# Performance work log

Hardware: AMD Instinct MI355X
Metric: run time of the kernel (lower is better)

## Reference

```python
import jax, jax.numpy as jnp
import numpy as np

N_NODES = 50000
N_EDGES = 500000
D = 128  # node/edge feature dim


def setup_inputs() -> dict:
    key = jax.random.key(0)
    k1, k2, k3, k4, k5 = jax.random.split(key, 5)
    x_node = jax.random.normal(k1, (N_NODES, D), dtype=jnp.float32)
    x_edge = jax.random.normal(k2, (N_EDGES, D), dtype=jnp.float32)
    edge_index = jax.random.randint(k3, (N_EDGES, 2), 0, N_NODES, dtype=jnp.int64)
    # MLP params: Linear(3D -> D) -> ReLU -> Linear(D -> D)
    W1 = jax.random.normal(k4, (3 * D, D), dtype=jnp.float32) * (1.0 / np.sqrt(3 * D))
    b1 = jnp.zeros((D,), dtype=jnp.float32)
    W2 = jax.random.normal(k5, (D, D), dtype=jnp.float32) * (1.0 / np.sqrt(D))
    b2 = jnp.zeros((D,), dtype=jnp.float32)
    return {"x_node": x_node, "x_edge": x_edge, "edge_index": edge_index,
            "W1": W1, "b1": b1, "W2": W2, "b2": b2}


def reference(x_node, x_edge, edge_index, W1, b1, W2, b2):
    # gather node features at both endpoints of each edge
    v0 = x_node[edge_index[:, 0]]          # [E, D]
    v1 = x_node[edge_index[:, 1]]          # [E, D]
    x_new = jnp.concatenate([v0, v1, x_edge], axis=1)  # [E, 3D]
    h = jax.nn.relu(x_new @ W1 + b1)       # [E, D]
    x_edge_new = h @ W2 + b2               # [E, D]
    return x_edge_new
```

## Files before the change

### kernel.cpp

```cpp
#include <hip/hip_runtime.h>
#include <stdint.h>

#define D 128
#define MT 64

typedef short short8 __attribute__((ext_vector_type(8)));
typedef float f32x16 __attribute__((ext_vector_type(16)));

__device__ __forceinline__ unsigned short f2bf(float f) {
    union { float f; uint32_t u; } v;
    v.f = f;
    uint32_t u = v.u;
    uint32_t r = (u + 0x7fffu + ((u >> 16) & 1u)) >> 16;
    return (unsigned short)r;
}

__global__ void pack_weights_kernel(const float* __restrict__ W1,
                                    const float* __restrict__ W2,
                                    unsigned short* __restrict__ W1p,
                                    unsigned short* __restrict__ W2p) {
    int t = blockIdx.x * 256 + threadIdx.x;
    if (t < 6144) {
        int kt = t >> 8, nt = (t >> 6) & 3, lane = t & 63;
        int n = nt * 32 + (lane & 31);
        int kb = kt * 16 + (lane >> 5) * 8;
        unsigned short* dst = W1p + t * 8;
        #pragma unroll
        for (int j = 0; j < 8; ++j) dst[j] = f2bf(W1[(kb + j) * D + n]);
    } else if (t < 8192) {
        int u = t - 6144;
        int kt = u >> 8, nt = (u >> 6) & 3, lane = u & 63;
        int n = nt * 32 + (lane & 31);
        int kb = kt * 16 + (lane >> 5) * 8;
        unsigned short* dst = W2p + u * 8;
        #pragma unroll
        for (int j = 0; j < 8; ++j) dst[j] = f2bf(W2[(kb + j) * D + n]);
    }
}

__global__ __launch_bounds__(256, 3) void edge_mlp_kernel(
    const float* __restrict__ x_node,
    const float* __restrict__ x_edge,
    const int* __restrict__ eidx,
    const unsigned short* __restrict__ W1p,
    const unsigned short* __restrict__ W2p,
    const float* __restrict__ b1,
    const float* __restrict__ b2,
    float* __restrict__ out,
    int E) {
    __shared__ unsigned short lds[MT * 392];
    unsigned short* Hs = lds;

    const int t = threadIdx.x;
    const int r0 = blockIdx.x * MT;

    {
        const int lane32 = t & 31;
        const int rsub = t >> 5;
        #pragma unroll
        for (int rb = 0; rb < 8; ++rb) {
            int row = rb * 8 + rsub;
            int rg = r0 + row;
            int rgc = rg < E ? rg : E - 1;
            int e0 = eidx[2 * rgc];
            int e1 = eidx[2 * rgc + 1];
            float4 v0 = ((const float4*)(x_node + (size_t)e0 * D))[lane32];
            float4 v1 = ((const float4*)(x_node + (size_t)e1 * D))[lane32];
            float4 v2 = ((const float4*)(x_edge + (size_t)rgc * D))[lane32];
            unsigned short* base = &lds[row * 392 + lane32 * 4];
            ushort4 p;
            p.x = f2bf(v0.x); p.y = f2bf(v0.y); p.z = f2bf(v0.z); p.w = f2bf(v0.w);
            *(ushort4*)(base) = p;
            p.x = f2bf(v1.x); p.y = f2bf(v1.y); p.z = f2bf(v1.z); p.w = f2bf(v1.w);
            *(ushort4*)(base + 128) = p;
            p.x = f2bf(v2.x); p.y = f2bf(v2.y); p.z = f2bf(v2.z); p.w = f2bf(v2.w);
            *(ushort4*)(base + 256) = p;
        }
    }
    __syncthreads();

    const int w = t >> 6;
    const int lane = t & 63;
    const int lrow = lane & 31;
    const int khalf = (lane >> 5) * 8;
    const int n = w * 32 + lrow;
    const int rbump = (lane >> 5) * 4;

    f32x16 acc0, acc1;
    #pragma unroll
    for (int i = 0; i < 16; ++i) { acc0[i] = 0.f; acc1[i] = 0.f; }

    for (int kt = 0; kt < 24; ++kt) {
        short8 a0 = *(const short8*)&lds[lrow * 392 + kt * 16 + khalf];
        short8 a1 = *(const short8*)&lds[(lrow + 32) * 392 + kt * 16 + khalf];
        short8 b  = *(const short8*)(W1p + ((kt * 4 + w) * 64 + lane) * 8);
        acc0 = __builtin_amdgcn_mfma_f32_32x32x16_bf16(a0, b, acc0, 0, 0, 0);
        acc1 = __builtin_amdgcn_mfma_f32_32x32x16_bf16(a1, b, acc1, 0, 0, 0);
    }
    __syncthreads();

    {
        float b1v = b1[n];
        #pragma unroll
        for (int r = 0; r < 16; ++r) {
            int rr = (r & 3) + 8 * (r >> 2) + rbump;
            float h0 = fmaxf(acc0[r] + b1v, 0.f);
            float h1 = fmaxf(acc1[r] + b1v, 0.f);
            Hs[rr * 136 + n] = f2bf(h0);
            Hs[(rr + 32) * 136 + n] = f2bf(h1);
        }
    }
    __syncthreads();

    f32x16 c0, c1;
    #pragma unroll
    for (int i = 0; i < 16; ++i) { c0[i] = 0.f; c1[i] = 0.f; }

    #pragma unroll
    for (int kt = 0; kt < 8; ++kt) {
        short8 a0 = *(const short8*)&Hs[lrow * 136 + kt * 16 + khalf];
        short8 a1 = *(const short8*)&Hs[(lrow + 32) * 136 + kt * 16 + khalf];
        short8 b  = *(const short8*)(W2p + ((kt * 4 + w) * 64 + lane) * 8);
        c0 = __builtin_amdgcn_mfma_f32_32x32x16_bf16(a0, b, c0, 0, 0, 0);
        c1 = __builtin_amdgcn_mfma_f32_32x32x16_bf16(a1, b, c1, 0, 0, 0);
    }

    {
        float b2v = b2[n];
        #pragma unroll
        for (int r = 0; r < 16; ++r) {
            int rr = (r & 3) + 8 * (r >> 2) + rbump;
            int rg = r0 + rr;
            if (rg < E) out[(size_t)rg * D + n] = c0[r] + b2v;
            if (rg + 32 < E) out[(size_t)(rg + 32) * D + n] = c1[r] + b2v;
        }
    }
}

extern "C" void kernel_launch(void* const* d_in, const int* in_sizes, int n_in,
                              void* d_out, int out_size, void* d_ws, size_t ws_size,
                              hipStream_t stream) {
    const float* x_node = (const float*)d_in[0];
    const float* x_edge = (const float*)d_in[1];
    const int*   eidx   = (const int*)d_in[2];
    const float* W1     = (const float*)d_in[3];
    const float* b1     = (const float*)d_in[4];
    const float* W2     = (const float*)d_in[5];
    const float* b2     = (const float*)d_in[6];
    float* out = (float*)d_out;

    const int E = in_sizes[1] / D;

    unsigned short* W1p = (unsigned short*)d_ws;
    unsigned short* W2p = W1p + 6144 * 8;

    pack_weights_kernel<<<32, 256, 0, stream>>>(W1, W2, W1p, W2p);

    int nblk = (E + MT - 1) / MT;
    edge_mlp_kernel<<<nblk, 256, 0, stream>>>(x_node, x_edge, eidx, W1p, W2p, b1, b2, out, E);
}
```

Measured before the change: 532.0 us.

## Halve edge tile, raise occupancy, preload MLP weights into registers

Shrinks the per-block edge tile from 64 to 32 rows and raises the launch-bounds occupancy target from 3 to 6 blocks. The aim is more resident waves to hide the latency of the random node gathers. All W1 and W2 bf16 fragments are loaded into registers at kernel start, and the biases are folded into the accumulator initialisation. The risk is register pressure: 32 short8 weight fragments plus accumulators are hard to fit under the tighter occupancy bound, so the compiler may spill. Halving the tile also doubles the number of times each block re-reads the weights from cache.

```diff
diff --git a/kernel.cpp b/kernel.cpp
--- a/kernel.cpp
+++ b/kernel.cpp
@@ -2,7 +2,7 @@
 #include <stdint.h>
 
 #define D 128
-#define MT 64
+#define MT 32
 
 typedef short short8 __attribute__((ext_vector_type(8)));
 typedef float f32x16 __attribute__((ext_vector_type(16)));
@@ -38,7 +38,7 @@
     }
 }
 
-__global__ __launch_bounds__(256, 3) void edge_mlp_kernel(
+__global__ __launch_bounds__(256, 6) void edge_mlp_kernel(
     const float* __restrict__ x_node,
     const float* __restrict__ x_edge,
     const int* __restrict__ eidx,
@@ -54,11 +54,29 @@
     const int t = threadIdx.x;
     const int r0 = blockIdx.x * MT;
 
+    const int w = t >> 6;
+    const int lane = t & 63;
+    const int lrow = lane & 31;
+    const int khalf = (lane >> 5) * 8;
+    const int n = w * 32 + lrow;
+    const int rbump = (lane >> 5) * 4;
+
+    short8 w1f[24];
+    #pragma unroll
+    for (int kt = 0; kt < 24; ++kt)
+        w1f[kt] = *(const short8*)(W1p + ((kt * 4 + w) * 64 + lane) * 8);
+    short8 w2f[8];
+    #pragma unroll
+    for (int kt = 0; kt < 8; ++kt)
+        w2f[kt] = *(const short8*)(W2p + ((kt * 4 + w) * 64 + lane) * 8);
+    const float b1v = b1[n];
+    const float b2v = b2[n];
+
     {
         const int lane32 = t & 31;
         const int rsub = t >> 5;
         #pragma unroll
-        for (int rb = 0; rb < 8; ++rb) {
+        for (int rb = 0; rb < 4; ++rb) {
             int row = rb * 8 + rsub;
             int rg = r0 + row;
             int rgc = rg < E ? rg : E - 1;
@@ -79,61 +97,39 @@
     }
     __syncthreads();
 
-    const int w = t >> 6;
-    const int lane = t & 63;
-    const int lrow = lane & 31;
-    const int khalf = (lane >> 5) * 8;
-    const int n = w * 32 + lrow;
-    const int rbump = (lane >> 5) * 4;
+    f32x16 acc;
+    #pragma unroll
+    for (int i = 0; i < 16; ++i) acc[i] = b1v;
 
-    f32x16 acc0, acc1;
     #pragma unroll
-    for (int i = 0; i < 16; ++i) { acc0[i] = 0.f; acc1[i] = 0.f; }
-
     for (int kt = 0; kt < 24; ++kt) {
-        short8 a0 = *(const short8*)&lds[lrow * 392 + kt * 16 + khalf];
-        short8 a1 = *(const short8*)&lds[(lrow + 32) * 392 + kt * 16 + khalf];
-        short8 b  = *(const short8*)(W1p + ((kt * 4 + w) * 64 + lane) * 8);
-        acc0 = __builtin_amdgcn_mfma_f32_32x32x16_bf16(a0, b, acc0, 0, 0, 0);
-        acc1 = __builtin_amdgcn_mfma_f32_32x32x16_bf16(a1, b, acc1, 0, 0, 0);
+        short8 a = *(const short8*)&lds[lrow * 392 + kt * 16 + khalf];
+        acc = __builtin_amdgcn_mfma_f32_32x32x16_bf16(a, w1f[kt], acc, 0, 0, 0);
     }
     __syncthreads();
 
-    {
-        float b1v = b1[n];
-        #pragma unroll
-        for (int r = 0; r < 16; ++r) {
-            int rr = (r & 3) + 8 * (r >> 2) + rbump;
-            float h0 = fmaxf(acc0[r] + b1v, 0.f);
-            float h1 = fmaxf(acc1[r] + b1v, 0.f);
-            Hs[rr * 136 + n] = f2bf(h0);
-            Hs[(rr + 32) * 136 + n] = f2bf(h1);
-        }
+    #pragma unroll
+    for (int r = 0; r < 16; ++r) {
+        int rr = (r & 3) + 8 * (r >> 2) + rbump;
+        Hs[rr * 136 + n] = f2bf(fmaxf(acc[r], 0.f));
     }
     __syncthreads();
 
-    f32x16 c0, c1;
+    f32x16 c;
     #pragma unroll
-    for (int i = 0; i < 16; ++i) { c0[i] = 0.f; c1[i] = 0.f; }
+    for (int i = 0; i < 16; ++i) c[i] = b2v;
 
     #pragma unroll
     for (int kt = 0; kt < 8; ++kt) {
-        short8 a0 = *(const short8*)&Hs[lrow * 136 + kt * 16 + khalf];
-        short8 a1 = *(const short8*)&Hs[(lrow + 32) * 136 + kt * 16 + khalf];
-        short8 b  = *(const short8*)(W2p + ((kt * 4 + w) * 64 + lane) * 8);
-        c0 = __builtin_amdgcn_mfma_f32_32x32x16_bf16(a0, b, c0, 0, 0, 0);
-        c1 = __builtin_amdgcn_mfma_f32_32x32x16_bf16(a1, b, c1, 0, 0, 0);
+        short8 a = *(const short8*)&Hs[lrow * 136 + kt * 16 + khalf];
+        c = __builtin_amdgcn_mfma_f32_32x32x16_bf16(a, w2f[kt], c, 0, 0, 0);
     }
 
-    {
-        float b2v = b2[n];
-        #pragma unroll
-        for (int r = 0; r < 16; ++r) {
-            int rr = (r & 3) + 8 * (r >> 2) + rbump;
-            int rg = r0 + rr;
-            if (rg < E) out[(size_t)rg * D + n] = c0[r] + b2v;
-            if (rg + 32 < E) out[(size_t)(rg + 32) * D + n] = c1[r] + b2v;
-        }
+    #pragma unroll
+    for (int r = 0; r < 16; ++r) {
+        int rr = (r & 3) + 8 * (r >> 2) + rbump;
+        int rg = r0 + rr;
+        if (rg < E) out[(size_t)rg * D + n] = c[r];
     }
 }
 
```

New measurement: 1.030 ms. +93.7%, slower.
